# Performance work log

Hardware: AMD Instinct MI355X
Metric: run time of the kernel (lower is better)

Reference implementation:

```python
import jax, jax.numpy as jnp
import numpy as np

D_STATE = 16
D_CONV = 4


def silu(x):
    return x * jax.nn.sigmoid(x)


def selective_scan(x, dt, A, Bm, Cm, Dp):
    # x, dt: (B,L,P); A: (P,N); Bm, Cm: (B,L,N); Dp: (P,)
    dA = jnp.exp(dt[..., None] * A)                    # (B,L,P,N)
    dBx = (dt * x)[..., None] * Bm[:, :, None, :]      # (B,L,P,N)

    def comb(c1, c2):
        a1, b1 = c1
        a2, b2 = c2
        return a1 * a2, a2 * b1 + b2

    _, h = jax.lax.associative_scan(comb, (dA, dBx), axis=1)
    y = jnp.einsum('blpn,bln->blp', h, Cm) + x * Dp
    return y


def mamba(seq, W_in, conv_w, conv_b, W_x, W_dt, b_dt, A_log, Dp, W_out):
    # seq: (B, L, D_model)
    xz = seq @ W_in.T                                  # (B,L,2P)
    P = xz.shape[-1] // 2
    x, z = xz[..., :P], xz[..., P:]
    # causal depthwise conv over L
    xc = jnp.transpose(x, (0, 2, 1))                   # (B,P,L)
    xc = jax.lax.conv_general_dilated(xc, conv_w[:, None, :], (1,),
                                      [(D_CONV - 1, 0)], feature_group_count=P)
    x = silu(jnp.transpose(xc, (0, 2, 1)) + conv_b)    # (B,L,P)
    proj = x @ W_x.T                                   # (B,L, dt_rank+2N)
    dtr = W_dt.shape[1]
    dt = jax.nn.softplus(proj[..., :dtr] @ W_dt.T + b_dt)
    Bm = proj[..., dtr:dtr + D_STATE]
    Cm = proj[..., dtr + D_STATE:]
    A = -jnp.exp(A_log)
    y = selective_scan(x, dt, A, Bm, Cm, Dp)
    y = y * silu(z)
    return y @ W_out.T                                 # (B,L,D_model)


def oss_forward(x1, x2, W_in, conv_w, conv_b, W_x, W_dt, b_dt, A_log, Dp, W_out):
    B, C, H, W = x1.shape
    L = H * W
    seq_h = jnp.transpose(x1.reshape(B, C, L), (0, 2, 1))                       # (B, H*W, C) row-major
    seq_w = jnp.transpose(jnp.transpose(x1, (0, 1, 3, 2)).reshape(B, C, L), (0, 2, 1))  # column-major

    def run(i, s):
        return mamba(s, W_in[i], conv_w[i], conv_b[i], W_x[i], W_dt[i],
                     b_dt[i], A_log[i], Dp[i], W_out[i])

    y_hf = run(0, seq_h)
    y_hb = jnp.flip(run(1, jnp.flip(seq_h, 1)), 1)
    y_wf = run(2, seq_w)
    y_wb = jnp.flip(run(3, jnp.flip(seq_w, 1)), 1)

    y_h = jnp.transpose((y_hf + y_hb).reshape(B, H, W, C), (0, 3, 1, 2))        # (B,C,H,W)
    y_w = jnp.transpose((y_wf + y_wb).reshape(B, W, H, C), (0, 3, 2, 1))        # (B,C,H,W)
    return y_h + y_w + x2


def setup_inputs() -> dict:
    key = jax.random.key(0)
    ks = jax.random.split(key, 12)
    B, C, H, W = 2, 96, 64, 64
    P = 2 * C            # d_inner = expand * d_model = 192
    N = D_STATE
    dtr = -(-C // 16)    # dt_rank = ceil(C/16) = 6
    s = 0.02
    inp = {
        'x1': jax.random.normal(ks[0], (B, C, H, W), jnp.float32),
        'x2': jax.random.normal(ks[1], (B, C, H, W), jnp.float32),
        'W_in': jax.random.normal(ks[2], (4, 2 * P, C), jnp.float32) * s,
        'conv_w': jax.random.normal(ks[3], (4, P, D_CONV), jnp.float32) * s,
        'conv_b': jnp.zeros((4, P), jnp.float32),
        'W_x': jax.random.normal(ks[4], (4, dtr + 2 * N, P), jnp.float32) * s,
        'W_dt': jax.random.normal(ks[5], (4, P, dtr), jnp.float32) * s,
        'b_dt': jax.random.normal(ks[6], (4, P), jnp.float32) * s,
        'A_log': jnp.log(jnp.tile(jnp.arange(1.0, N + 1.0, dtype=jnp.float32), (4, P, 1))),
        'Dp': jnp.ones((4, P), jnp.float32),
        'W_out': jax.random.normal(ks[7], (4, C, P), jnp.float32) * s,
    }
    return inp


def reference(x1, x2, W_in, conv_w, conv_b, W_x, W_dt, b_dt, A_log, Dp, W_out):
    return oss_forward(x1, x2, W_in, conv_w, conv_b, W_x, W_dt, b_dt, A_log, Dp, W_out)
```

## Files before the change

kernel.cpp:

```cpp
#include <hip/hip_runtime.h>

#define D_DIRS 4
#define BB 2
#define CC 96
#define LL 4096
#define PP 192
#define TWOP 384
#define NN 16
#define DTR 6
#define NPROJ 38
#define NCH 256
#define CLEN 16
#define SEQT 24576

typedef __bf16 bf16x8 __attribute__((ext_vector_type(8)));
typedef float f32x4 __attribute__((ext_vector_type(4)));

__device__ __forceinline__ float fast_softplus(float v) {
    return fmaxf(v, 0.0f) + __logf(1.0f + __expf(-fabsf(v)));
}

__global__ void k_prep(const float* __restrict__ W_in, const float* __restrict__ W_x,
                       const float* __restrict__ W_out, __bf16* __restrict__ wbin,
                       __bf16* __restrict__ wbx, __bf16* __restrict__ wbout)
{
    int i = blockIdx.x * 256 + threadIdx.x;
    const int n0 = 4 * 384 * 104, n1 = 4 * 48 * 200, n2 = 4 * 96 * 200;
    if (i < n0) {
        int c = i % 104, jd = i / 104;
        wbin[i] = (c < 96) ? (__bf16)W_in[jd * 96 + c] : (__bf16)0.0f;
    } else if (i < n0 + n1) {
        int k = i - n0;
        int c = k % 200, jd = k / 200;
        int d = jd / 48, j = jd - d * 48;
        float v = (j < 38 && c < 192) ? W_x[(d * 38 + j) * 192 + c] : 0.0f;
        wbx[k] = (__bf16)v;
    } else if (i < n0 + n1 + n2) {
        int k = i - n0 - n1;
        int c = k % 200, jd = k / 200;
        float v = (c < 192) ? W_out[jd * 192 + c] : 0.0f;
        wbout[k] = (__bf16)v;
    }
}

__global__ __launch_bounds__(256) void k_img(
    const float* __restrict__ x1, __bf16* __restrict__ imgH, __bf16* __restrict__ imgW)
{
    __shared__ float t[96 * 65];
    const int b = blockIdx.y;
    const int lt = blockIdx.x;
    const int tid = threadIdx.x;
    for (int i = tid; i < 96 * 64; i += 256) {
        int c = i >> 6, lw = i & 63;
        t[c * 65 + lw] = x1[((b * 96 + c) << 12) + (lt << 6) + lw];
    }
    __syncthreads();
    for (int i = tid; i < 64 * 12; i += 256) {
        int lw = i / 12, q = i - lw * 12;
        union { __bf16 h[8]; uint4 u; } pk;
#pragma unroll
        for (int j = 0; j < 8; ++j) pk.h[j] = (__bf16)t[(q * 8 + j) * 65 + lw];
        ((uint4*)(imgH + (long)((b << 12) + (lt << 6) + lw) * 104))[q] = pk.u;
        ((uint4*)(imgW + (long)((b << 12) + (lw << 6) + lt) * 104))[q] = pk.u;
    }
}

__global__ __launch_bounds__(256) void k_gemm_in(
    const __bf16* __restrict__ imgH, const __bf16* __restrict__ imgW,
    const __bf16* __restrict__ wbin, float* __restrict__ xz_x, __bf16* __restrict__ zb)
{
    __shared__ __align__(16) __bf16 As[64 * 104];
    __shared__ __align__(16) __bf16 Bs[64 * 104];
    const int db = blockIdx.y;
    const int d = db >> 1, b = db & 1;
    const int t0 = blockIdx.x * 64;
    const int tid = threadIdx.x;
    const __bf16* img = (d < 2 ? imgH : imgW) + (long)b * (LL * 104);

    {
        uint4* adst = (uint4*)As;
        for (int i = tid; i < 832; i += 256) {
            int r = i / 13, q = i - r * 13;
            int l = (d & 1) ? (LL - 1 - (t0 + r)) : (t0 + r);
            adst[i] = ((const uint4*)(img + (long)l * 104))[q];
        }
    }

    const int lane = tid & 63;
    const int w = tid >> 6;
    const int wm = (w >> 1) * 32, wn = (w & 1) * 32;
    const int lr = lane & 15, lk = (lane >> 4) * 8;
    const int orow = (lane >> 4) * 4;

    for (int j0 = 0; j0 < TWOP; j0 += 64) {
        __syncthreads();
        {
            const uint4* bsrc = (const uint4*)(wbin + (long)(d * TWOP + j0) * 104);
            uint4* bdst = (uint4*)Bs;
            for (int i = tid; i < 832; i += 256) bdst[i] = bsrc[i];
        }
        __syncthreads();

        f32x4 acc[2][2] = {{{0.f,0.f,0.f,0.f},{0.f,0.f,0.f,0.f}},
                           {{0.f,0.f,0.f,0.f},{0.f,0.f,0.f,0.f}}};
#pragma unroll
        for (int ks = 0; ks < 96; ks += 32) {
            bf16x8 a0 = *(const bf16x8*)&As[(wm + lr) * 104 + ks + lk];
            bf16x8 a1 = *(const bf16x8*)&As[(wm + 16 + lr) * 104 + ks + lk];
            bf16x8 b0 = *(const bf16x8*)&Bs[(wn + lr) * 104 + ks + lk];
            bf16x8 b1 = *(const bf16x8*)&Bs[(wn + 16 + lr) * 104 + ks + lk];
            acc[0][0] = __builtin_amdgcn_mfma_f32_16x16x32_bf16(a0, b0, acc[0][0], 0, 0, 0);
            acc[0][1] = __builtin_amdgcn_mfma_f32_16x16x32_bf16(a0, b1, acc[0][1], 0, 0, 0);
            acc[1][0] = __builtin_amdgcn_mfma_f32_16x16x32_bf16(a1, b0, acc[1][0], 0, 0, 0);
            acc[1][1] = __builtin_amdgcn_mfma_f32_16x16x32_bf16(a1, b1, acc[1][1], 0, 0, 0);
        }
#pragma unroll
        for (int mi = 0; mi < 2; ++mi)
#pragma unroll
            for (int ni = 0; ni < 2; ++ni) {
                long mbase = (long)(db * LL + t0 + wm + mi * 16 + orow);
                int jcol = j0 + wn + ni * 16 + lr;
                if (j0 < PP) {
#pragma unroll
                    for (int r = 0; r < 4; ++r) xz_x[(mbase + r) * PP + jcol] = acc[mi][ni][r];
                } else {
#pragma unroll
                    for (int r = 0; r < 4; ++r) zb[(mbase + r) * PP + jcol - PP] = (__bf16)acc[mi][ni][r];
                }
            }
    }
}

__global__ __launch_bounds__(192) void k_conv(
    const float* __restrict__ xz_x, const float* __restrict__ conv_w,
    const float* __restrict__ conv_b, __bf16* __restrict__ xb16)
{
    __shared__ float xs[67 * 192];
    const int db = blockIdx.y;
    const int t0 = blockIdx.x * 64;
    const int d = db >> 1;
    const int m0 = db * LL + t0;
    const int tid = threadIdx.x;

    const float4* src = (const float4*)(xz_x + ((long)m0 - 3) * PP);
    for (int i = tid; i < 67 * 48; i += 192) {
        float4 v;
        if (t0 == 0 && i < 144) v = make_float4(0.f, 0.f, 0.f, 0.f);
        else v = src[i];
        ((float4*)xs)[i] = v;
    }

    const int p = tid;
    const float* wp = conv_w + (d * PP + p) * 4;
    float w0 = wp[0], w1 = wp[1], w2 = wp[2], w3 = wp[3];
    float bias = conv_b[d * PP + p];
    __syncthreads();

    for (int t = 0; t < 64; ++t) {
        float acc = bias + w0 * xs[t * PP + p] + w1 * xs[(t + 1) * PP + p]
                         + w2 * xs[(t + 2) * PP + p] + w3 * xs[(t + 3) * PP + p];
        float s = acc / (1.0f + __expf(-acc));
        xb16[(long)(m0 + t) * 200 + p] = (__bf16)s;
    }
}

__global__ __launch_bounds__(256) void k_gemm_proj(
    const __bf16* __restrict__ xb16, const __bf16* __restrict__ wbx, float* __restrict__ proj)
{
    __shared__ __align__(16) __bf16 As[64 * 200];
    __shared__ __align__(16) __bf16 Bs[48 * 200];
    const int m0 = blockIdx.x * 64;
    const int d = m0 >> 13;
    const int tid = threadIdx.x;

    for (int i = tid; i < 1600; i += 256) {
        int r = i / 25, q = i - r * 25;
        ((uint4*)As)[i] = ((const uint4*)(xb16 + (long)(m0 + r) * 200))[q];
    }
    {
        const uint4* bsrc = (const uint4*)(wbx + (long)d * 48 * 200);
        uint4* bdst = (uint4*)Bs;
        for (int i = tid; i < 1200; i += 256) bdst[i] = bsrc[i];
    }
    __syncthreads();

    const int lane = tid & 63;
    const int w = tid >> 6;
    const int lr = lane & 15, lk = (lane >> 4) * 8;
    const int orow = (lane >> 4) * 4;

    f32x4 acc[3] = {{0.f,0.f,0.f,0.f},{0.f,0.f,0.f,0.f},{0.f,0.f,0.f,0.f}};
#pragma unroll
    for (int ks = 0; ks < 192; ks += 32) {
        bf16x8 a = *(const bf16x8*)&As[(w * 16 + lr) * 200 + ks + lk];
#pragma unroll
        for (int ni = 0; ni < 3; ++ni) {
            bf16x8 bfr = *(const bf16x8*)&Bs[(ni * 16 + lr) * 200 + ks + lk];
            acc[ni] = __builtin_amdgcn_mfma_f32_16x16x32_bf16(a, bfr, acc[ni], 0, 0, 0);
        }
    }
#pragma unroll
    for (int ni = 0; ni < 3; ++ni) {
        int j = ni * 16 + lr;
        if (j < NPROJ) {
#pragma unroll
            for (int r = 0; r < 4; ++r) {
                int m = m0 + w * 16 + orow + r;
                proj[(long)m * NPROJ + j] = acc[ni][r];
            }
        }
    }
}

__global__ __launch_bounds__(256) void k_gemm_out(
    const __bf16* __restrict__ ysb, const __bf16* __restrict__ wbout, float* __restrict__ yo)
{
    __shared__ __align__(16) __bf16 As[64 * 200];
    __shared__ __align__(16) __bf16 Bs[96 * 200];
    const int m0 = blockIdx.x * 64;
    const int d = m0 >> 13;
    const int tid = threadIdx.x;

    for (int i = tid; i < 1600; i += 256) {
        int r = i / 25, q = i - r * 25;
        ((uint4*)As)[i] = ((const uint4*)(ysb + (long)(m0 + r) * 200))[q];
    }
    {
        const uint4* bsrc = (const uint4*)(wbout + (long)d * 96 * 200);
        uint4* bdst = (uint4*)Bs;
        for (int i = tid; i < 2400; i += 256) bdst[i] = bsrc[i];
    }
    __syncthreads();

    const int lane = tid & 63;
    const int w = tid >> 6;
    const int wm = (w >> 1) * 32, wn = (w & 1) * 48;
    const int lr = lane & 15, lk = (lane >> 4) * 8;
    const int orow = (lane >> 4) * 4;

    f32x4 acc[2][3] = {};
#pragma unroll
    for (int ks = 0; ks < 192; ks += 32) {
        bf16x8 a0 = *(const bf16x8*)&As[(wm + lr) * 200 + ks + lk];
        bf16x8 a1 = *(const bf16x8*)&As[(wm + 16 + lr) * 200 + ks + lk];
#pragma unroll
        for (int ni = 0; ni < 3; ++ni) {
            bf16x8 bfr = *(const bf16x8*)&Bs[(wn + ni * 16 + lr) * 200 + ks + lk];
            acc[0][ni] = __builtin_amdgcn_mfma_f32_16x16x32_bf16(a0, bfr, acc[0][ni], 0, 0, 0);
            acc[1][ni] = __builtin_amdgcn_mfma_f32_16x16x32_bf16(a1, bfr, acc[1][ni], 0, 0, 0);
        }
    }
#pragma unroll
    for (int mi = 0; mi < 2; ++mi)
#pragma unroll
        for (int ni = 0; ni < 3; ++ni) {
#pragma unroll
            for (int r = 0; r < 4; ++r) {
                int m = m0 + wm + mi * 16 + orow + r;
                yo[(long)m * CC + wn + ni * 16 + lr] = acc[mi][ni][r];
            }
        }
}

__global__ __launch_bounds__(192) void k_pass1(
    const __bf16* __restrict__ xb16, const float* __restrict__ proj,
    const float* __restrict__ A_log, const float* __restrict__ W_dt,
    const float* __restrict__ b_dt,
    float* __restrict__ cb_pa, float* __restrict__ cb_h)
{
    __shared__ __align__(16) float pl[CLEN * 40];
    __shared__ __align__(16) __bf16 xsb[CLEN * 200];
    const int tid = threadIdx.x;
    const int chunk = blockIdx.x;
    const int db = blockIdx.y;
    const int d = db >> 1;
    const int m0 = db * LL + chunk * CLEN;

    const float* pr = proj + (long)m0 * NPROJ;
    for (int i = tid; i < CLEN * NPROJ; i += 192) {
        int r = i / NPROJ, c = i - r * NPROJ;
        int col = (c < 6) ? c : c + 2;
        pl[r * 40 + col] = pr[i];
    }
    for (int i = tid; i < 400; i += 192) {
        int r = i / 25, q = i - r * 25;
        ((uint4*)xsb)[i] = ((const uint4*)(xb16 + (long)(m0 + r) * 200))[q];
    }

    const int p = tid;
    float A[16];
    {
        const float4* al4 = reinterpret_cast<const float4*>(A_log + (d * PP + p) * NN);
#pragma unroll
        for (int q = 0; q < 4; ++q) {
            float4 a = al4[q];
            A[4*q]   = -__expf(a.x); A[4*q+1] = -__expf(a.y);
            A[4*q+2] = -__expf(a.z); A[4*q+3] = -__expf(a.w);
        }
    }
    float w[6];
    const float* wd = W_dt + (d * PP + p) * DTR;
#pragma unroll
    for (int r = 0; r < 6; ++r) w[r] = wd[r];
    const float bdt = b_dt[d * PP + p];
    float h[16];
#pragma unroll
    for (int n = 0; n < 16; ++n) h[n] = 0.f;
    float sdt = 0.f;
    __syncthreads();

#pragma unroll
    for (int s = 0; s < CLEN; ++s) {
        const float* row = pl + s * 40;
        float4 d0 = *(const float4*)(row);
        float4 d1 = *(const float4*)(row + 4);
        float v = bdt + d0.x*w[0] + d0.y*w[1] + d0.z*w[2] + d0.w*w[3] + d1.x*w[4] + d1.y*w[5];
        float dtv = fast_softplus(v);
        sdt += dtv;
        float dtx = dtv * (float)xsb[s * 200 + p];
        const float4* B4 = reinterpret_cast<const float4*>(row + 8);
#pragma unroll
        for (int q = 0; q < 4; ++q) {
            float4 Bv = B4[q];
            h[4*q+0] = __expf(dtv * A[4*q+0])*h[4*q+0] + dtx*Bv.x;
            h[4*q+1] = __expf(dtv * A[4*q+1])*h[4*q+1] + dtx*Bv.y;
            h[4*q+2] = __expf(dtv * A[4*q+2])*h[4*q+2] + dtx*Bv.z;
            h[4*q+3] = __expf(dtv * A[4*q+3])*h[4*q+3] + dtx*Bv.w;
        }
    }
    const long cbase = (long)chunk * SEQT + db * PP + p;
#pragma unroll
    for (int n = 0; n < 16; ++n) {
        cb_pa[cbase + n * 1536] = __expf(A[n] * sdt);
        cb_h [cbase + n * 1536] = h[n];
    }
}

__global__ void k_chunkscan(const float* __restrict__ cb_pa, float* __restrict__ cb_h)
{
    int j = blockIdx.x * 256 + threadIdx.x;
    float run = 0.0f;
    for (int c = 0; c < NCH; c += 8) {
        float pa[8], hh[8];
#pragma unroll
        for (int i = 0; i < 8; ++i) {
            long o = (long)(c + i) * SEQT + j;
            pa[i] = cb_pa[o]; hh[i] = cb_h[o];
        }
#pragma unroll
        for (int i = 0; i < 8; ++i) {
            cb_h[(long)(c + i) * SEQT + j] = run;
            run = pa[i] * run + hh[i];
        }
    }
}

__global__ __launch_bounds__(192) void k_pass2(
    const __bf16* __restrict__ xb16, const float* __restrict__ proj,
    const float* __restrict__ A_log, const float* __restrict__ W_dt,
    const float* __restrict__ b_dt, const float* __restrict__ Dp,
    const __bf16* __restrict__ zb, const float* __restrict__ cb_h,
    __bf16* __restrict__ ysb)
{
    __shared__ __align__(16) float pl[CLEN * 40];
    __shared__ __align__(16) __bf16 xsb[CLEN * 200];
    __shared__ __align__(16) __bf16 zs[CLEN * PP];
    const int tid = threadIdx.x;
    const int chunk = blockIdx.x;
    const int db = blockIdx.y;
    const int d = db >> 1;
    const int m0 = db * LL + chunk * CLEN;

    const float* pr = proj + (long)m0 * NPROJ;
    for (int i = tid; i < CLEN * NPROJ; i += 192) {
        int r = i / NPROJ, c = i - r * NPROJ;
        int col = (c < 6) ? c : c + 2;
        pl[r * 40 + col] = pr[i];
    }
    for (int i = tid; i < 400; i += 192) {
        int r = i / 25, q = i - r * 25;
        ((uint4*)xsb)[i] = ((const uint4*)(xb16 + (long)(m0 + r) * 200))[q];
    }
    {
        const uint4* zsrc = reinterpret_cast<const uint4*>(zb + (long)m0 * PP);
        uint4* zdst = reinterpret_cast<uint4*>(zs);
        zdst[tid] = zsrc[tid];
        zdst[tid + 192] = zsrc[tid + 192];
    }

    const int p = tid;
    float A[16];
    {
        const float4* al4 = reinterpret_cast<const float4*>(A_log + (d * PP + p) * NN);
#pragma unroll
        for (int q = 0; q < 4; ++q) {
            float4 a = al4[q];
            A[4*q]   = -__expf(a.x); A[4*q+1] = -__expf(a.y);
            A[4*q+2] = -__expf(a.z); A[4*q+3] = -__expf(a.w);
        }
    }
    float w[6];
    const float* wd = W_dt + (d * PP + p) * DTR;
#pragma unroll
    for (int r = 0; r < 6; ++r) w[r] = wd[r];
    const float bdt = b_dt[d * PP + p];
    const float Dv = Dp[d * PP + p];

    float h[16];
    const long cbase = (long)chunk * SEQT + db * PP + p;
#pragma unroll
    for (int n = 0; n < 16; ++n) h[n] = cb_h[cbase + n * 1536];
    __syncthreads();

#pragma unroll
    for (int s = 0; s < CLEN; ++s) {
        const float* row = pl + s * 40;
        float4 d0 = *(const float4*)(row);
        float4 d1 = *(const float4*)(row + 4);
        float v = bdt + d0.x*w[0] + d0.y*w[1] + d0.z*w[2] + d0.w*w[3] + d1.x*w[4] + d1.y*w[5];
        float dtv = fast_softplus(v);
        float xvv = (float)xsb[s * 200 + p];
        float dtx = dtv * xvv;
        const float4* B4 = reinterpret_cast<const float4*>(row + 8);
        const float4* C4 = reinterpret_cast<const float4*>(row + 24);
        float y = 0.0f;
#pragma unroll
        for (int q = 0; q < 4; ++q) {
            float4 Bv = B4[q];
            float4 Cv = C4[q];
            h[4*q+0] = __expf(dtv * A[4*q+0])*h[4*q+0] + dtx*Bv.x; y += h[4*q+0]*Cv.x;
            h[4*q+1] = __expf(dtv * A[4*q+1])*h[4*q+1] + dtx*Bv.y; y += h[4*q+1]*Cv.y;
            h[4*q+2] = __expf(dtv * A[4*q+2])*h[4*q+2] + dtx*Bv.z; y += h[4*q+2]*Cv.z;
            h[4*q+3] = __expf(dtv * A[4*q+3])*h[4*q+3] + dtx*Bv.w; y += h[4*q+3]*Cv.w;
        }
        float zvv = (float)zs[s * PP + p];
        ysb[(long)(m0 + s) * 200 + p] = (__bf16)((y + xvv * Dv) * (zvv / (1.0f + __expf(-zvv))));
    }
}

__global__ void k_final(const float* __restrict__ x2, const float* __restrict__ yo,
                        float* __restrict__ out)
{
    int idx = blockIdx.x * blockDim.x + threadIdx.x;
    const int total = BB * CC * LL;
    for (; idx < total; idx += gridDim.x * blockDim.x) {
        int w = idx & 63;
        int h = (idx >> 6) & 63;
        int c = (idx >> 12) % CC;
        int b = idx / (CC * LL);
        int lh = (h << 6) | w;
        int lw = (w << 6) | h;
        long m0 = (long)(0 * BB + b) * LL + lh;
        long m1 = (long)(1 * BB + b) * LL + (LL - 1 - lh);
        long m2 = (long)(2 * BB + b) * LL + lw;
        long m3 = (long)(3 * BB + b) * LL + (LL - 1 - lw);
        out[idx] = x2[idx] + yo[m0 * CC + c] + yo[m1 * CC + c] + yo[m2 * CC + c] + yo[m3 * CC + c];
    }
}

extern "C" void kernel_launch(void* const* d_in, const int* in_sizes, int n_in,
                              void* d_out, int out_size, void* d_ws, size_t ws_size,
                              hipStream_t stream)
{
    const float* x1     = (const float*)d_in[0];
    const float* x2     = (const float*)d_in[1];
    const float* W_in   = (const float*)d_in[2];
    const float* conv_w = (const float*)d_in[3];
    const float* conv_b = (const float*)d_in[4];
    const float* W_x    = (const float*)d_in[5];
    const float* W_dt   = (const float*)d_in[6];
    const float* b_dt   = (const float*)d_in[7];
    const float* A_log  = (const float*)d_in[8];
    const float* Dp     = (const float*)d_in[9];
    const float* W_out  = (const float*)d_in[10];
    float* out = (float*)d_out;
    float* ws  = (float*)d_ws;

    float*  xz_x  = ws;
    __bf16* zb    = (__bf16*)(ws + 6291456);
    __bf16* xb16  = (__bf16*)(ws + 9437184);
    float*  proj  = ws + 12713984;
    float*  cb_pa = ws + 13959168;
    float*  cb_h  = ws + 20250624;
    __bf16* imgH  = (__bf16*)(ws + 26542080);
    __bf16* imgW  = (__bf16*)(ws + 26968064);
    __bf16* wbin  = (__bf16*)(ws + 27394048);
    __bf16* wbx   = (__bf16*)(ws + 27473920);
    __bf16* wbout = (__bf16*)(ws + 27493120);
    __bf16* ysb = (__bf16*)xz_x;
    float*  yo  = cb_pa;

    k_prep<<<dim3(1074), 256, 0, stream>>>(W_in, W_x, W_out, wbin, wbx, wbout);
    k_img<<<dim3(64, 2), 256, 0, stream>>>(x1, imgH, imgW);
    k_gemm_in<<<dim3(64, 8), 256, 0, stream>>>(imgH, imgW, wbin, xz_x, zb);
    k_conv<<<dim3(64, 8), 192, 0, stream>>>(xz_x, conv_w, conv_b, xb16);
    k_gemm_proj<<<dim3(512), 256, 0, stream>>>(xb16, wbx, proj);
    k_pass1<<<dim3(NCH, 8), 192, 0, stream>>>(xb16, proj, A_log, W_dt, b_dt, cb_pa, cb_h);
    k_chunkscan<<<dim3(SEQT / 256), 256, 0, stream>>>(cb_pa, cb_h);
    k_pass2<<<dim3(NCH, 8), 192, 0, stream>>>(xb16, proj, A_log, W_dt, b_dt, Dp, zb, cb_h, ysb);
    k_gemm_out<<<dim3(512), 256, 0, stream>>>(ysb, wbout, yo);
    k_final<<<dim3(3072), 256, 0, stream>>>(x2, yo, out);
}
```

Measured before the change: 157.4 us.

## Split scan state dimension across thread pairs and use exp2 in chunk passes

Both chunked scan passes now run 384 threads per block, with each channel's 16 state entries split across two adjacent threads holding 8 each. Pass 2 combines the partial C·h dot products with a lane shuffle, and only the even lane writes the output. Exponentials are rewritten as exp2 with log2(e) folded into A. The split doubles thread-level parallelism and halves per-thread register pressure and serial exp work, at the cost of duplicated softplus and dt computation in each thread pair and idle lanes on the output write.

```diff
diff --git a/kernel.cpp b/kernel.cpp
--- a/kernel.cpp
+++ b/kernel.cpp
@@ -12,6 +12,7 @@
 #define NCH 256
 #define CLEN 16
 #define SEQT 24576
+#define LOG2E 1.44269504088896340736f
 
 typedef __bf16 bf16x8 __attribute__((ext_vector_type(8)));
 typedef float f32x4 __attribute__((ext_vector_type(4)));
@@ -262,7 +263,7 @@
         }
 }
 
-__global__ __launch_bounds__(192) void k_pass1(
+__global__ __launch_bounds__(384) void k_pass1(
     const __bf16* __restrict__ xb16, const float* __restrict__ proj,
     const float* __restrict__ A_log, const float* __restrict__ W_dt,
     const float* __restrict__ b_dt,
@@ -277,25 +278,27 @@
     const int m0 = db * LL + chunk * CLEN;
 
     const float* pr = proj + (long)m0 * NPROJ;
-    for (int i = tid; i < CLEN * NPROJ; i += 192) {
+    for (int i = tid; i < CLEN * NPROJ; i += 384) {
         int r = i / NPROJ, c = i - r * NPROJ;
         int col = (c < 6) ? c : c + 2;
         pl[r * 40 + col] = pr[i];
     }
-    for (int i = tid; i < 400; i += 192) {
+    for (int i = tid; i < 400; i += 384) {
         int r = i / 25, q = i - r * 25;
         ((uint4*)xsb)[i] = ((const uint4*)(xb16 + (long)(m0 + r) * 200))[q];
     }
 
-    const int p = tid;
-    float A[16];
+    const int p = tid >> 1;
+    const int half = tid & 1;
+    const int nb = half * 8;
+    float A2[8];
     {
-        const float4* al4 = reinterpret_cast<const float4*>(A_log + (d * PP + p) * NN);
-#pragma unroll
-        for (int q = 0; q < 4; ++q) {
+        const float4* al4 = (const float4*)(A_log + (d * PP + p) * NN + nb);
+#pragma unroll
+        for (int q = 0; q < 2; ++q) {
             float4 a = al4[q];
-            A[4*q]   = -__expf(a.x); A[4*q+1] = -__expf(a.y);
-            A[4*q+2] = -__expf(a.z); A[4*q+3] = -__expf(a.w);
+            A2[4*q]   = -__expf(a.x) * LOG2E; A2[4*q+1] = -__expf(a.y) * LOG2E;
+            A2[4*q+2] = -__expf(a.z) * LOG2E; A2[4*q+3] = -__expf(a.w) * LOG2E;
         }
     }
     float w[6];
@@ -303,9 +306,9 @@
 #pragma unroll
     for (int r = 0; r < 6; ++r) w[r] = wd[r];
     const float bdt = b_dt[d * PP + p];
-    float h[16];
-#pragma unroll
-    for (int n = 0; n < 16; ++n) h[n] = 0.f;
+    float h[8];
+#pragma unroll
+    for (int n = 0; n < 8; ++n) h[n] = 0.f;
     float sdt = 0.f;
     __syncthreads();
 
@@ -318,21 +321,21 @@
         float dtv = fast_softplus(v);
         sdt += dtv;
         float dtx = dtv * (float)xsb[s * 200 + p];
-        const float4* B4 = reinterpret_cast<const float4*>(row + 8);
-#pragma unroll
-        for (int q = 0; q < 4; ++q) {
+        const float4* B4 = (const float4*)(row + 8 + nb);
+#pragma unroll
+        for (int q = 0; q < 2; ++q) {
             float4 Bv = B4[q];
-            h[4*q+0] = __expf(dtv * A[4*q+0])*h[4*q+0] + dtx*Bv.x;
-            h[4*q+1] = __expf(dtv * A[4*q+1])*h[4*q+1] + dtx*Bv.y;
-            h[4*q+2] = __expf(dtv * A[4*q+2])*h[4*q+2] + dtx*Bv.z;
-            h[4*q+3] = __expf(dtv * A[4*q+3])*h[4*q+3] + dtx*Bv.w;
+            h[4*q+0] = exp2f(dtv * A2[4*q+0])*h[4*q+0] + dtx*Bv.x;
+            h[4*q+1] = exp2f(dtv * A2[4*q+1])*h[4*q+1] + dtx*Bv.y;
+            h[4*q+2] = exp2f(dtv * A2[4*q+2])*h[4*q+2] + dtx*Bv.z;
+            h[4*q+3] = exp2f(dtv * A2[4*q+3])*h[4*q+3] + dtx*Bv.w;
         }
     }
     const long cbase = (long)chunk * SEQT + db * PP + p;
 #pragma unroll
-    for (int n = 0; n < 16; ++n) {
-        cb_pa[cbase + n * 1536] = __expf(A[n] * sdt);
-        cb_h [cbase + n * 1536] = h[n];
+    for (int n = 0; n < 8; ++n) {
+        cb_pa[cbase + (nb + n) * 1536] = exp2f(A2[n] * sdt);
+        cb_h [cbase + (nb + n) * 1536] = h[n];
     }
 }
 
@@ -355,7 +358,7 @@
     }
 }
 
-__global__ __launch_bounds__(192) void k_pass2(
+__global__ __launch_bounds__(384) void k_pass2(
     const __bf16* __restrict__ xb16, const float* __restrict__ proj,
     const float* __restrict__ A_log, const float* __restrict__ W_dt,
     const float* __restrict__ b_dt, const float* __restrict__ Dp,
@@ -372,31 +375,31 @@
     const int m0 = db * LL + chunk * CLEN;
 
     const float* pr = proj + (long)m0 * NPROJ;
-    for (int i = tid; i < CLEN * NPROJ; i += 192) {
+    for (int i = tid; i < CLEN * NPROJ; i += 384) {
         int r = i / NPROJ, c = i - r * NPROJ;
         int col = (c < 6) ? c : c + 2;
         pl[r * 40 + col] = pr[i];
     }
-    for (int i = tid; i < 400; i += 192) {
+    for (int i = tid; i < 400; i += 384) {
         int r = i / 25, q = i - r * 25;
         ((uint4*)xsb)[i] = ((const uint4*)(xb16 + (long)(m0 + r) * 200))[q];
     }
+    if (tid < 384) {
+        const uint4* zsrc = (const uint4*)(zb + (long)m0 * PP);
+        ((uint4*)zs)[tid] = zsrc[tid];
+    }
+
+    const int p = tid >> 1;
+    const int half = tid & 1;
+    const int nb = half * 8;
+    float A2[8];
     {
-        const uint4* zsrc = reinterpret_cast<const uint4*>(zb + (long)m0 * PP);
-        uint4* zdst = reinterpret_cast<uint4*>(zs);
-        zdst[tid] = zsrc[tid];
-        zdst[tid + 192] = zsrc[tid + 192];
-    }
-
-    const int p = tid;
-    float A[16];
-    {
-        const float4* al4 = reinterpret_cast<const float4*>(A_log + (d * PP + p) * NN);
-#pragma unroll
-        for (int q = 0; q < 4; ++q) {
+        const float4* al4 = (const float4*)(A_log + (d * PP + p) * NN + nb);
+#pragma unroll
+        for (int q = 0; q < 2; ++q) {
             float4 a = al4[q];
-            A[4*q]   = -__expf(a.x); A[4*q+1] = -__expf(a.y);
-            A[4*q+2] = -__expf(a.z); A[4*q+3] = -__expf(a.w);
+            A2[4*q]   = -__expf(a.x) * LOG2E; A2[4*q+1] = -__expf(a.y) * LOG2E;
+            A2[4*q+2] = -__expf(a.z) * LOG2E; A2[4*q+3] = -__expf(a.w) * LOG2E;
         }
     }
     float w[6];
@@ -406,10 +409,10 @@
     const float bdt = b_dt[d * PP + p];
     const float Dv = Dp[d * PP + p];
 
-    float h[16];
+    float h[8];
     const long cbase = (long)chunk * SEQT + db * PP + p;
 #pragma unroll
-    for (int n = 0; n < 16; ++n) h[n] = cb_h[cbase + n * 1536];
+    for (int n = 0; n < 8; ++n) h[n] = cb_h[cbase + (nb + n) * 1536];
     __syncthreads();
 
 #pragma unroll
@@ -421,20 +424,23 @@
         float dtv = fast_softplus(v);
         float xvv = (float)xsb[s * 200 + p];
         float dtx = dtv * xvv;
-        const float4* B4 = reinterpret_cast<const float4*>(row + 8);
-        const float4* C4 = reinterpret_cast<const float4*>(row + 24);
+        const float4* B4 = (const float4*)(row + 8 + nb);
+        const float4* C4 = (const float4*)(row + 24 + nb);
         float y = 0.0f;
 #pragma unroll
-        for (int q = 0; q < 4; ++q) {
+        for (int q = 0; q < 2; ++q) {
             float4 Bv = B4[q];
             float4 Cv = C4[q];
-            h[4*q+0] = __expf(dtv * A[4*q+0])*h[4*q+0] + dtx*Bv.x; y += h[4*q+0]*Cv.x;
-            h[4*q+1] = __expf(dtv * A[4*q+1])*h[4*q+1] + dtx*Bv.y; y += h[4*q+1]*Cv.y;
-            h[4*q+2] = __expf(dtv * A[4*q+2])*h[4*q+2] + dtx*Bv.z; y += h[4*q+2]*Cv.z;
-            h[4*q+3] = __expf(dtv * A[4*q+3])*h[4*q+3] + dtx*Bv.w; y += h[4*q+3]*Cv.w;
-        }
-        float zvv = (float)zs[s * PP + p];
-        ysb[(long)(m0 + s) * 200 + p] = (__bf16)((y + xvv * Dv) * (zvv / (1.0f + __expf(-zvv))));
+            h[4*q+0] = exp2f(dtv * A2[4*q+0])*h[4*q+0] + dtx*Bv.x; y += h[4*q+0]*Cv.x;
+            h[4*q+1] = exp2f(dtv * A2[4*q+1])*h[4*q+1] + dtx*Bv.y; y += h[4*q+1]*Cv.y;
+            h[4*q+2] = exp2f(dtv * A2[4*q+2])*h[4*q+2] + dtx*Bv.z; y += h[4*q+2]*Cv.z;
+            h[4*q+3] = exp2f(dtv * A2[4*q+3])*h[4*q+3] + dtx*Bv.w; y += h[4*q+3]*Cv.w;
+        }
+        y += __shfl_xor(y, 1);
+        if (half == 0) {
+            float zvv = (float)zs[s * PP + p];
+            ysb[(long)(m0 + s) * 200 + p] = (__bf16)((y + xvv * Dv) * (zvv / (1.0f + __expf(-zvv))));
+        }
     }
 }
 
@@ -495,9 +501,9 @@
     k_gemm_in<<<dim3(64, 8), 256, 0, stream>>>(imgH, imgW, wbin, xz_x, zb);
     k_conv<<<dim3(64, 8), 192, 0, stream>>>(xz_x, conv_w, conv_b, xb16);
     k_gemm_proj<<<dim3(512), 256, 0, stream>>>(xb16, wbx, proj);
-    k_pass1<<<dim3(NCH, 8), 192, 0, stream>>>(xb16, proj, A_log, W_dt, b_dt, cb_pa, cb_h);
+    k_pass1<<<dim3(NCH, 8), 384, 0, stream>>>(xb16, proj, A_log, W_dt, b_dt, cb_pa, cb_h);
     k_chunkscan<<<dim3(SEQT / 256), 256, 0, stream>>>(cb_pa, cb_h);
-    k_pass2<<<dim3(NCH, 8), 192, 0, stream>>>(xb16, proj, A_log, W_dt, b_dt, Dp, zb, cb_h, ysb);
+    k_pass2<<<dim3(NCH, 8), 384, 0, stream>>>(xb16, proj, A_log, W_dt, b_dt, Dp, zb, cb_h, ysb);
     k_gemm_out<<<dim3(512), 256, 0, stream>>>(ysb, wbout, yo);
     k_final<<<dim3(3072), 256, 0, stream>>>(x2, yo, out);
 }
```

After: 189.6 us. +20.4%, slower.
